# Performance work log

Measured on AMD Instinct MI355X. Metric: run time of the kernel, lower is better.

## Reference

```python
import jax, jax.numpy as jnp
import numpy as np

N, E, G, H = 100000, 1600000, 256, 2
EPS = 1e-5


def _gat_conv(x, src, dst, W, a_src, a_dst, bias, C):
    # PyG GATConv (concat=True, negative_slope=0.2): lin has no bias, bias added after concat.
    h = (x @ W).reshape(N, H, C)                                   # [N,H,C]
    e_src = (h * a_src).sum(-1)                                    # [N,H]
    e_dst = (h * a_dst).sum(-1)                                    # [N,H]
    alpha = jax.nn.leaky_relu(e_src[src] + e_dst[dst], 0.2)        # [Etot,H]
    amax = jax.ops.segment_max(alpha, dst, num_segments=N)         # segment softmax over incoming edges
    ex = jnp.exp(alpha - amax[dst])
    denom = jax.ops.segment_sum(ex, dst, num_segments=N)
    msg = h[src] * ex[:, :, None]                                  # [Etot,H,C]
    out = jax.ops.segment_sum(msg, dst, num_segments=N) / (denom[:, :, None] + 1e-16)
    return out.reshape(N, H * C) + bias


def _bn(x, g, b, m, v):  # BatchNorm in eval mode with running stats
    return g * (x - m) * jax.lax.rsqrt(v + EPS) + b


def _forward(edge_index, batch, x, w1, as1, ad1, b1, g1, be1, m1, v1, p1w, p1b,
             w2, as2, ad2, b2, g2, be2, m2, v2, p2w, p2b,
             w3, as3, ad3, b3, g3, be3, m3, v3, p3w, p3b,
             fw, fb, g4, be4, m4, v4, l1w, l1b, l2w, l2b):
    loops = jnp.arange(N, dtype=edge_index.dtype)                  # GATConv add_self_loops=True
    src = jnp.concatenate([edge_index[0], loops])
    dst = jnp.concatenate([edge_index[1], loops])
    h = jax.nn.relu(_bn(_gat_conv(x, src, dst, w1, as1, ad1, b1, 32), g1, be1, m1, v1)) + (x @ p1w + p1b)
    h = jax.nn.relu(_bn(_gat_conv(h, src, dst, w2, as2, ad2, b2, 64), g2, be2, m2, v2)) + (h @ p2w + p2b)
    h = jax.nn.relu(_bn(_gat_conv(h, src, dst, w3, as3, ad3, b3, 64), g3, be3, m3, v3)) + (h @ p3w + p3b)
    counts = jax.ops.segment_sum(jnp.ones((N,), h.dtype), batch, num_segments=G)
    pooled = jax.ops.segment_sum(h, batch, num_segments=G) / jnp.maximum(counts, 1.0)[:, None]  # [G,128]
    z = jax.nn.relu(_bn(pooled @ fw + fb, g4, be4, m4, v4))
    z = jax.nn.relu(z @ l1w + l1b)
    return z @ l2w + l2b                                           # [G,10]


def setup_inputs():
    key = jax.random.key(0)
    ks = jax.random.split(key, 48)
    it = iter(range(48))
    def rn(shape, s=0.1):
        return jax.random.normal(ks[next(it)], shape, jnp.float32) * s
    def bn_params(dim):  # gamma, beta, running_mean, running_var
        return (jax.random.uniform(ks[next(it)], (dim,), jnp.float32, 0.5, 1.5),
                rn((dim,)), rn((dim,)),
                jax.random.uniform(ks[next(it)], (dim,), jnp.float32, 0.5, 1.5))
    inp = {}
    inp["x"] = jax.random.normal(ks[next(it)], (N, 5), jnp.float32)
    inp["edge_index"] = jax.random.randint(ks[next(it)], (2, E), 0, N, jnp.int32)
    inp["batch"] = jnp.sort(jax.random.randint(ks[next(it)], (N,), 0, G, jnp.int32))
    inp["w1"], inp["as1"], inp["ad1"], inp["b1"] = rn((5, 64)), rn((H, 32)), rn((H, 32)), rn((64,))
    inp["g1"], inp["be1"], inp["m1"], inp["v1"] = bn_params(64)
    inp["p1w"], inp["p1b"] = rn((5, 64)), rn((64,))
    inp["w2"], inp["as2"], inp["ad2"], inp["b2"] = rn((64, 128)), rn((H, 64)), rn((H, 64)), rn((128,))
    inp["g2"], inp["be2"], inp["m2"], inp["v2"] = bn_params(128)
    inp["p2w"], inp["p2b"] = rn((64, 128)), rn((128,))
    inp["w3"], inp["as3"], inp["ad3"], inp["b3"] = rn((128, 128)), rn((H, 64)), rn((H, 64)), rn((128,))
    inp["g3"], inp["be3"], inp["m3"], inp["v3"] = bn_params(128)
    inp["p3w"], inp["p3b"] = rn((128, 128)), rn((128,))
    inp["fw"], inp["fb"] = rn((128, 32)), rn((32,))
    inp["g4"], inp["be4"], inp["m4"], inp["v4"] = bn_params(32)
    inp["l1w"], inp["l1b"] = rn((32, 32)), rn((32,))
    inp["l2w"], inp["l2b"] = rn((32, 10)), rn((10,))
    return inp


def reference(x, edge_index, batch, w1, as1, ad1, b1, g1, be1, m1, v1, p1w, p1b,
              w2, as2, ad2, b2, g2, be2, m2, v2, p2w, p2b,
              w3, as3, ad3, b3, g3, be3, m3, v3, p3w, p3b,
              fw, fb, g4, be4, m4, v4, l1w, l1b, l2w, l2b):
    return _forward(edge_index, batch, x, w1, as1, ad1, b1, g1, be1, m1, v1, p1w, p1b,
                    w2, as2, ad2, b2, g2, be2, m2, v2, p2w, p2b,
                    w3, as3, ad3, b3, g3, be3, m3, v3, p3w, p3b,
                    fw, fb, g4, be4, m4, v4, l1w, l1b, l2w, l2b)
```

## Files before the change

### kernel.cpp

```cpp
#include <hip/hip_runtime.h>
#include <hip/hip_bf16.h>
#include <hip/hip_fp16.h>

#define NN   100000
#define EE   1600000
#define ETOT (EE + NN)
#define GG   256
#define BNEPS 1e-5f
#define NBK  391
#define PADTOT (ETOT + NBK * 4096 + 64)
#define PSPLIT 16

typedef float floatx2 __attribute__((ext_vector_type(2)));
typedef short s16x8 __attribute__((ext_vector_type(8)));
typedef float f32x4v __attribute__((ext_vector_type(4)));

__device__ __forceinline__ unsigned short f2bf(float f) {
    unsigned u = __float_as_uint(f);
    unsigned r = u + 0x7FFF + ((u >> 16) & 1);
    return (unsigned short)(r >> 16);
}
__device__ __forceinline__ float bf2f(unsigned short b) {
    return __uint_as_float(((unsigned)b) << 16);
}
__device__ __forceinline__ floatx2 pkfma(floatx2 a, floatx2 b, floatx2 c) {
    return __builtin_elementwise_fma(a, b, c);
}


__global__ __launch_bounds__(256) void bucket_count_kernel(
    const int* __restrict__ ei, int* __restrict__ bucket_cnt)
{
    __shared__ int cnt[NBK];
    for (int i = threadIdx.x; i < NBK; i += 256) cnt[i] = 0;
    __syncthreads();
    int base = blockIdx.x * 8192;
    for (int k = threadIdx.x; k < 8192; k += 256) {
        int e = base + k;
        if (e < ETOT) {
            int dst = (e < EE) ? ei[EE + e] : (e - EE);
            atomicAdd(&cnt[dst >> 8], 1);
        }
    }
    __syncthreads();
    for (int i = threadIdx.x; i < NBK; i += 256)
        if (cnt[i]) atomicAdd(&bucket_cnt[i], cnt[i]);
}

__global__ __launch_bounds__(512) void bucket_scan_kernel(
    const int* __restrict__ bucket_cnt, int* __restrict__ bucket_base,
    int* __restrict__ gcursor, float* __restrict__ esrcs)
{
    __shared__ int s[512];
    int t = threadIdx.x;
    int v = (t < NBK) ? bucket_cnt[t] : 0;
    s[t] = v;
    __syncthreads();
    int x = v;
    for (int o = 1; o < 512; o <<= 1) {
        int y = (t >= o) ? s[t - o] : 0;
        __syncthreads();
        x += y;
        s[t] = x;
        __syncthreads();
    }
    if (t < NBK) { bucket_base[t] = x - v; gcursor[t] = x - v; }
    if (t == 0) {
        bucket_base[NBK] = ETOT;
        esrcs[2 * NN]     = __int_as_float(0xFF800000);
        esrcs[2 * NN + 1] = __int_as_float(0xFF800000);
    }
}

__global__ __launch_bounds__(256) void partition_kernel(
    const int* __restrict__ ei, int* __restrict__ gcursor, int* __restrict__ part)
{
    __shared__ int cnt[NBK];
    __shared__ int basel[NBK];
    for (int i = threadIdx.x; i < NBK; i += 256) cnt[i] = 0;
    __syncthreads();
    int base = blockIdx.x * 4096;
    for (int k = threadIdx.x; k < 4096; k += 256) {
        int e = base + k;
        if (e < ETOT) {
            int dst = (e < EE) ? ei[EE + e] : (e - EE);
            atomicAdd(&cnt[dst >> 8], 1);
        }
    }
    __syncthreads();
    for (int i = threadIdx.x; i < NBK; i += 256) {
        int c = cnt[i];
        basel[i] = c ? atomicAdd(&gcursor[i], c) : 0;
        cnt[i] = 0;
    }
    __syncthreads();
    for (int k = threadIdx.x; k < 4096; k += 256) {
        int e = base + k;
        if (e < ETOT) {
            int src, dst;
            if (e < EE) { src = ei[e]; dst = ei[EE + e]; }
            else        { src = e - EE; dst = e - EE; }
            int b = dst >> 8;
            int slot = atomicAdd(&cnt[b], 1);
            part[basel[b] + slot] = src | ((dst & 255) << 17);
        }
    }
}

__global__ __launch_bounds__(256) void csr_build_kernel(
    const int* __restrict__ part, const int* __restrict__ bucket_base,
    int* __restrict__ row2_start, int* __restrict__ row2_deg,
    int* __restrict__ csr2_src)
{
    __shared__ int degs[256];
    __shared__ int sc[256];
    __shared__ int cur[256];
    int b = blockIdx.x;
    int t = threadIdx.x;
    int beg = bucket_base[b], end = bucket_base[b + 1];
    int pbase = ((beg + 7) & ~7) + 4096 * b;
    degs[t] = 0;
    __syncthreads();
    for (int j = beg + t; j < end; j += 256)
        atomicAdd(&degs[(part[j] >> 17) & 255], 1);
    __syncthreads();
    int dg = degs[t];
    int pdeg = (dg + 7) & ~7;
    sc[t] = pdeg;
    __syncthreads();
    int x = pdeg;
    for (int o = 1; o < 256; o <<= 1) {
        int y = (t >= o) ? sc[t - o] : 0;
        __syncthreads();
        x += y;
        sc[t] = x;
        __syncthreads();
    }
    int start2 = pbase + (x - pdeg);
    int node = b * 256 + t;
    if (node < NN) { row2_start[node] = start2; row2_deg[node] = dg; }
    cur[t] = start2;
    __syncthreads();
    for (int j = beg + t; j < end; j += 256) {
        int pv = part[j];
        int pos = atomicAdd(&cur[(pv >> 17) & 255], 1);
        csr2_src[pos] = pv & 0x1FFFF;
    }
    for (int k = dg; k < pdeg; ++k) csr2_src[start2 + k] = NN;
}


template<int K>
__device__ __forceinline__ void prep_w_body(
    int unit, const float* __restrict__ W, const float* __restrict__ pw,
    short* __restrict__ wfrag)
{
    constexpr int KS = K / 32;
    int total = 16 * KS * 2 * 64;
    if (unit >= total) return;
    int lane = unit & 63;
    int rest = unit >> 6;
    int hilo = rest & 1;
    int fk = rest >> 1;
    int ks = fk % KS;
    int nt = fk / KS;
    int n = nt * 16 + (lane & 15);
    int k0 = ks * 32 + (lane >> 4) * 8;
    const float* src = (n < 128) ? (W + n) : (pw + (n - 128));
    s16x8 out;
#pragma unroll
    for (int j = 0; j < 8; ++j) {
        float wv = src[(size_t)(k0 + j) * 128];
        unsigned short hi = f2bf(wv);
        if (hilo == 0) {
            out[j] = (short)hi;
        } else {
            float fhi = __uint_as_float(((unsigned)hi) << 16);
            out[j] = (short)f2bf(wv - fhi);
        }
    }
    *(s16x8*)(wfrag + (size_t)unit * 8) = out;
}

__global__ __launch_bounds__(256) void prep_all_kernel(
    const float* __restrict__ w2, const float* __restrict__ p2w, short* __restrict__ wfrag2,
    const float* __restrict__ w3, const float* __restrict__ p3w, short* __restrict__ wfrag3,
    const float* b1, const float* g1, const float* be1, const float* m1, const float* v1,
    const float* b2, const float* g2, const float* be2, const float* m2, const float* v2,
    const float* b3, const float* g3, const float* be3, const float* m3, const float* v3,
    float* sc1, float* sh1, float* sc2, float* sh2, float* sc3, float* sh3)
{
    int b = blockIdx.x;
    int tid = threadIdx.x;
    if (b < 16) {
        prep_w_body<64>(b * 256 + tid, w2, p2w, wfrag2);
    } else if (b < 48) {
        prep_w_body<128>((b - 16) * 256 + tid, w3, p3w, wfrag3);
    } else {
        int t = tid;
        if (t < 128) {
            if (t < 64) {
                float sc = g1[t] * rsqrtf(v1[t] + BNEPS);
                sc1[t] = sc;
                sh1[t] = (b1[t] - m1[t]) * sc + be1[t];
            }
            {
                float sc = g2[t] * rsqrtf(v2[t] + BNEPS);
                sc2[t] = sc;
                sh2[t] = (b2[t] - m2[t]) * sc + be2[t];
            }
            {
                float sc = g3[t] * rsqrtf(v3[t] + BNEPS);
                sc3[t] = sc;
                sh3[t] = (b3[t] - m3[t]) * sc + be3[t];
            }
        }
    }
}


__global__ __launch_bounds__(256) void edgew_kernel(
    const int* __restrict__ csr2_src, const int* __restrict__ row2_start,
    const int* __restrict__ row2_deg,
    const float2* __restrict__ esrc, const float2* __restrict__ edst,
    unsigned* __restrict__ csr_w, int nN)
{
    int n = blockIdx.x * 4 + (threadIdx.x >> 6);
    int lane = threadIdx.x & 63;
    if (n >= nN) return;
    float2 ed = edst[n];
    int s2 = row2_start[n];
    int dg = row2_deg[n];
    int pc = (dg + 7) & ~7;
    for (int j = lane; j < pc; j += 64) {
        int i = csr2_src[s2 + j];
        float2 es = esrc[i];
        float a0 = es.x + ed.x; a0 = (a0 > 0.f) ? a0 : 0.2f * a0;
        float a1 = es.y + ed.y; a1 = (a1 > 0.f) ? a1 : 0.2f * a1;
        unsigned w = (unsigned)f2bf(__expf(a0)) | ((unsigned)f2bf(__expf(a1)) << 16);
        csr_w[s2 + j] = w;
    }
}


__global__ __launch_bounds__(256) void feat1_kernel(
    const float* __restrict__ xin, const float* __restrict__ W,
    const float* __restrict__ pw, const float* __restrict__ pb,
    const float* __restrict__ a_src, const float* __restrict__ a_dst,
    unsigned char* __restrict__ h8, float* __restrict__ esrc, float* __restrict__ edst,
    unsigned short* __restrict__ rout16, int nN)
{
    constexpr int F_IN = 5, F_OUT = 64;
    int t = threadIdx.x;
    int n = blockIdx.x * 4 + t / F_OUT;
    int f = t % F_OUT;
    if (n >= nN) return;
    float acc = 0.f, racc = 0.f;
#pragma unroll
    for (int k = 0; k < F_IN; ++k) {
        float xv = xin[n * F_IN + k];
        acc  += xv * W[k * F_OUT + f];
        racc += xv * pw[k * F_OUT + f];
    }
    float other = __shfl_xor(acc, 1, 64);
    if ((f & 1) == 0) {
        int p = __builtin_amdgcn_cvt_pk_fp8_f32(acc, other, 0, false);
        *(unsigned short*)(h8 + (size_t)n * F_OUT + f) = (unsigned short)(p & 0xFFFF);
    }
    rout16[(size_t)n * F_OUT + f] = f2bf(racc + pb[f]);
    float es = acc * a_src[f];
    float ed = acc * a_dst[f];
#pragma unroll
    for (int off = 16; off > 0; off >>= 1) {
        es += __shfl_xor(es, off, 32);
        ed += __shfl_xor(ed, off, 32);
    }
    if ((t & 31) == 0) {
        int head = (f >> 5) & 1;
        esrc[n * 2 + head] = es;
        edst[n * 2 + head] = ed;
    }
}


template<int K>
__global__ __launch_bounds__(512) void mfma_feat_kernel(
    const unsigned short* __restrict__ xin16, const short* __restrict__ wfrag,
    const float* __restrict__ pb,
    const float* __restrict__ a_src, const float* __restrict__ a_dst,
    unsigned char* __restrict__ h8, float* __restrict__ esrc, float* __restrict__ edst,
    unsigned short* __restrict__ rout16)
{
    constexpr int KS = K / 32;
    constexpr int CH = K / 8;
    __shared__ __align__(16) char smem[53248];
    s16x8* xs = (s16x8*)smem;
    unsigned short* h8lds = (unsigned short*)smem;
    unsigned short* rolds = (unsigned short*)(smem + 18432);

    const int tid = threadIdx.x;
    const int base = blockIdx.x * 128;

    for (int idx = tid; idx < 128 * CH; idx += 512) {
        int node = idx / CH;
        int ch = idx % CH;
        int gn = base + node; if (gn > NN - 1) gn = NN - 1;
        s16x8 v = *(const s16x8*)(xin16 + (size_t)gn * K + ch * 8);
        int tt = node >> 4, mm = node & 15;
        xs[(tt * CH + ch) * 16 + mm] = v;
    }
    __syncthreads();

    const int w = tid >> 6;
    const int lane = tid & 63;
    const int quad = lane >> 4;
    const int m = lane & 15;
    const int l0 = w * 16 + quad * 4;
    const int node0 = base + l0;

    s16x8 a0[KS];
#pragma unroll
    for (int ks = 0; ks < KS; ++ks)
        a0[ks] = xs[(w * CH + (ks * 4 + quad)) * 16 + m];
    __syncthreads();

    float esh0[4] = {0.f,0.f,0.f,0.f}, esh1[4] = {0.f,0.f,0.f,0.f};
    float edh0[4] = {0.f,0.f,0.f,0.f}, edh1[4] = {0.f,0.f,0.f,0.f};

#pragma unroll
    for (int nt = 0; nt < 16; ++nt) {
        s16x8 b[2 * KS];
#pragma unroll
        for (int i = 0; i < 2 * KS; ++i)
            b[i] = *(const s16x8*)(wfrag + (size_t)((nt * KS * 2 + i) * 64 + lane) * 8);
        f32x4v c0 = {0.f, 0.f, 0.f, 0.f};
#pragma unroll
        for (int ks = 0; ks < KS; ++ks) {
            c0 = __builtin_amdgcn_mfma_f32_16x16x32_bf16(a0[ks], b[2 * ks + 0], c0, 0, 0, 0);
            c0 = __builtin_amdgcn_mfma_f32_16x16x32_bf16(a0[ks], b[2 * ks + 1], c0, 0, 0, 0);
        }
        if (nt < 8) {
            int col = nt * 16 + m;
            float av = a_src[col], dv = a_dst[col];
#pragma unroll
            for (int r = 0; r < 4; ++r) {
                float v0 = c0[r];
                if (nt < 4) {
                    esh0[r] = fmaf(v0, av, esh0[r]); edh0[r] = fmaf(v0, dv, edh0[r]);
                } else {
                    esh1[r] = fmaf(v0, av, esh1[r]); edh1[r] = fmaf(v0, dv, edh1[r]);
                }
                float p0 = __shfl_xor(v0, 1, 16);
                if ((m & 1) == 0) {
                    int us = nt * 8 + (m >> 1);
                    int pk0 = __builtin_amdgcn_cvt_pk_fp8_f32(v0, p0, 0, false);
                    h8lds[(l0 + r) * 72 + us] = (unsigned short)(pk0 & 0xFFFF);
                }
            }
        } else {
            int col = (nt - 8) * 16 + m;
            float bv = pb[col];
#pragma unroll
            for (int r = 0; r < 4; ++r)
                rolds[(l0 + r) * 136 + col] = f2bf(c0[r] + bv);
        }
    }

#pragma unroll
    for (int r = 0; r < 4; ++r) {
#pragma unroll
        for (int off = 8; off > 0; off >>= 1) {
            esh0[r] += __shfl_xor(esh0[r], off, 16);
            esh1[r] += __shfl_xor(esh1[r], off, 16);
            edh0[r] += __shfl_xor(edh0[r], off, 16);
            edh1[r] += __shfl_xor(edh1[r], off, 16);
        }
    }
    if (m == 0) {
#pragma unroll
        for (int r = 0; r < 4; ++r) {
            if (node0 + r < NN) {
                ((float2*)esrc)[node0 + r] = make_float2(esh0[r], esh1[r]);
                ((float2*)edst)[node0 + r] = make_float2(edh0[r], edh1[r]);
            }
        }
    }

    __syncthreads();
    for (int i = tid; i < 128 * 8; i += 512) {
        int row = i >> 3, ch = i & 7;
        int node = base + row;
        if (node < NN) {
            int4 v = *(const int4*)(smem + row * 144 + ch * 16);
            *(int4*)(h8 + (size_t)node * 128 + ch * 16) = v;
        }
    }
    for (int i = tid; i < 128 * 16; i += 512) {
        int row = i >> 4, ch = i & 15;
        int node = base + row;
        if (node < NN) {
            int4 v = *(const int4*)(smem + 18432 + row * 272 + ch * 16);
            *(int4*)((char*)rout16 + (size_t)node * 256 + ch * 16) = v;
        }
    }
}


__global__ __launch_bounds__(256) void aggregate128_kernel(
    const unsigned char* __restrict__ h8,
    const int* __restrict__ row2_start, const int* __restrict__ row2_deg,
    const int* __restrict__ csr2_src, const unsigned* __restrict__ csr_w,
    const float* __restrict__ bnsc, const float* __restrict__ bnsh,
    unsigned short* __restrict__ io16)
{
    int w = threadIdx.x >> 6;
    int lane = threadIdx.x & 63;
    int half = lane >> 5;
    int fl = lane & 31;
    unsigned shl = (fl >= 16) ? 0u : 16u;
    int n = blockIdx.x * 8 + w * 2 + half;
    int s2 = row2_start[n];
    int dg = row2_deg[n];
    int pc = (dg + 7) & ~7;
    const int4* sp = (const int4*)(csr2_src + s2);
    const uint4* wp = (const uint4*)(csr_w + s2);
    float s = 0.f;
    floatx2 acc01 = {0.f, 0.f}, acc23 = {0.f, 0.f};
    for (int j = 0; j < pc; j += 8) {
        int4 ia = sp[(j >> 2) + 0];
        int4 ib = sp[(j >> 2) + 1];
        uint4 wa = wp[(j >> 2) + 0];
        uint4 wb = wp[(j >> 2) + 1];
        unsigned d0 = *(const unsigned*)(h8 + (size_t)ia.x * 128 + fl * 4);
        unsigned d1 = *(const unsigned*)(h8 + (size_t)ia.y * 128 + fl * 4);
        unsigned d2 = *(const unsigned*)(h8 + (size_t)ia.z * 128 + fl * 4);
        unsigned d3 = *(const unsigned*)(h8 + (size_t)ia.w * 128 + fl * 4);
        unsigned d4 = *(const unsigned*)(h8 + (size_t)ib.x * 128 + fl * 4);
        unsigned d5 = *(const unsigned*)(h8 + (size_t)ib.y * 128 + fl * 4);
        unsigned d6 = *(const unsigned*)(h8 + (size_t)ib.z * 128 + fl * 4);
        unsigned d7 = *(const unsigned*)(h8 + (size_t)ib.w * 128 + fl * 4);
        float g0 = __uint_as_float((wa.x << shl) & 0xFFFF0000u);
        float g1 = __uint_as_float((wa.y << shl) & 0xFFFF0000u);
        float g2 = __uint_as_float((wa.z << shl) & 0xFFFF0000u);
        float g3 = __uint_as_float((wa.w << shl) & 0xFFFF0000u);
        float g4 = __uint_as_float((wb.x << shl) & 0xFFFF0000u);
        float g5 = __uint_as_float((wb.y << shl) & 0xFFFF0000u);
        float g6 = __uint_as_float((wb.z << shl) & 0xFFFF0000u);
        float g7 = __uint_as_float((wb.w << shl) & 0xFFFF0000u);
        floatx2 gv0 = {g0, g0};
        floatx2 gv1 = {g1, g1};
        floatx2 gv2 = {g2, g2};
        floatx2 gv3 = {g3, g3};
        floatx2 gv4 = {g4, g4};
        floatx2 gv5 = {g5, g5};
        floatx2 gv6 = {g6, g6};
        floatx2 gv7 = {g7, g7};
        acc01 = pkfma(gv0, __builtin_amdgcn_cvt_pk_f32_fp8((int)d0, false), acc01);
        acc23 = pkfma(gv0, __builtin_amdgcn_cvt_pk_f32_fp8((int)d0, true),  acc23);
        acc01 = pkfma(gv1, __builtin_amdgcn_cvt_pk_f32_fp8((int)d1, false), acc01);
        acc23 = pkfma(gv1, __builtin_amdgcn_cvt_pk_f32_fp8((int)d1, true),  acc23);
        acc01 = pkfma(gv2, __builtin_amdgcn_cvt_pk_f32_fp8((int)d2, false), acc01);
        acc23 = pkfma(gv2, __builtin_amdgcn_cvt_pk_f32_fp8((int)d2, true),  acc23);
        acc01 = pkfma(gv3, __builtin_amdgcn_cvt_pk_f32_fp8((int)d3, false), acc01);
        acc23 = pkfma(gv3, __builtin_amdgcn_cvt_pk_f32_fp8((int)d3, true),  acc23);
        acc01 = pkfma(gv4, __builtin_amdgcn_cvt_pk_f32_fp8((int)d4, false), acc01);
        acc23 = pkfma(gv4, __builtin_amdgcn_cvt_pk_f32_fp8((int)d4, true),  acc23);
        acc01 = pkfma(gv5, __builtin_amdgcn_cvt_pk_f32_fp8((int)d5, false), acc01);
        acc23 = pkfma(gv5, __builtin_amdgcn_cvt_pk_f32_fp8((int)d5, true),  acc23);
        acc01 = pkfma(gv6, __builtin_amdgcn_cvt_pk_f32_fp8((int)d6, false), acc01);
        acc23 = pkfma(gv6, __builtin_amdgcn_cvt_pk_f32_fp8((int)d6, true),  acc23);
        acc01 = pkfma(gv7, __builtin_amdgcn_cvt_pk_f32_fp8((int)d7, false), acc01);
        acc23 = pkfma(gv7, __builtin_amdgcn_cvt_pk_f32_fp8((int)d7, true),  acc23);
        s += (((g0 + g1) + (g2 + g3)) + ((g4 + g5) + (g6 + g7)));
    }
    float inv = 1.f / (s + 1e-16f);
    int f0 = fl * 4;
    float4 sc = *(const float4*)(bnsc + f0);
    float4 sh = *(const float4*)(bnsh + f0);
    float o0 = fmaf(acc01.x * inv, sc.x, sh.x);
    float o1 = fmaf(acc01.y * inv, sc.y, sh.y);
    float o2 = fmaf(acc23.x * inv, sc.z, sh.z);
    float o3 = fmaf(acc23.y * inv, sc.w, sh.w);
    uint2* iop = (uint2*)(io16 + (size_t)n * 128 + f0);
    uint2 pu = *iop;
    float r0 = fmaxf(o0, 0.f) + __uint_as_float((pu.x & 0xFFFFu) << 16);
    float r1 = fmaxf(o1, 0.f) + __uint_as_float(pu.x & 0xFFFF0000u);
    float r2 = fmaxf(o2, 0.f) + __uint_as_float((pu.y & 0xFFFFu) << 16);
    float r3 = fmaxf(o3, 0.f) + __uint_as_float(pu.y & 0xFFFF0000u);
    uint2 ov;
    ov.x = (unsigned)f2bf(r0) | ((unsigned)f2bf(r1) << 16);
    ov.y = (unsigned)f2bf(r2) | ((unsigned)f2bf(r3) << 16);
    *iop = ov;
}


__global__ __launch_bounds__(256) void aggregate64_kernel(
    const unsigned char* __restrict__ h8,
    const int* __restrict__ row2_start, const int* __restrict__ row2_deg,
    const int* __restrict__ csr2_src, const unsigned* __restrict__ csr_w,
    const float* __restrict__ bnsc, const float* __restrict__ bnsh,
    unsigned short* __restrict__ io16)
{
    int w = threadIdx.x >> 6;
    int lane = threadIdx.x & 63;
    int half = lane >> 5;
    int hl = lane & 31;
    int q  = hl >> 4;
    int fl = hl & 15;
    unsigned shl = (fl >= 8) ? 0u : 16u;
    int n = blockIdx.x * 8 + w * 2 + half;
    int s2 = row2_start[n];
    int dg = row2_deg[n];
    int pc = (dg + 7) & ~7;
    const int4* sp = (const int4*)(csr2_src + s2);
    const uint4* wp = (const uint4*)(csr_w + s2);
    float s = 0.f;
    floatx2 acc01 = {0.f, 0.f}, acc23 = {0.f, 0.f};
    for (int j = 0; j < pc; j += 8) {
        int4 ia = sp[(j >> 2) + 0];
        int4 ib = sp[(j >> 2) + 1];
        uint4 wa = wp[(j >> 2) + 0];
        uint4 wb = wp[(j >> 2) + 1];
        int i0 = q ? ia.y : ia.x;
        int i1 = q ? ia.w : ia.z;
        int i2 = q ? ib.y : ib.x;
        int i3 = q ? ib.w : ib.z;
        unsigned w0 = q ? wa.y : wa.x;
        unsigned w1 = q ? wa.w : wa.z;
        unsigned w2 = q ? wb.y : wb.x;
        unsigned w3 = q ? wb.w : wb.z;
        unsigned d0 = *(const unsigned*)(h8 + (size_t)i0 * 64 + fl * 4);
        unsigned d1 = *(const unsigned*)(h8 + (size_t)i1 * 64 + fl * 4);
        unsigned d2 = *(const unsigned*)(h8 + (size_t)i2 * 64 + fl * 4);
        unsigned d3 = *(const unsigned*)(h8 + (size_t)i3 * 64 + fl * 4);
        float g0 = __uint_as_float((w0 << shl) & 0xFFFF0000u);
        float g1 = __uint_as_float((w1 << shl) & 0xFFFF0000u);
        float g2 = __uint_as_float((w2 << shl) & 0xFFFF0000u);
        float g3 = __uint_as_float((w3 << shl) & 0xFFFF0000u);
        floatx2 gv0 = {g0, g0};
        floatx2 gv1 = {g1, g1};
        floatx2 gv2 = {g2, g2};
        floatx2 gv3 = {g3, g3};
        acc01 = pkfma(gv0, __builtin_amdgcn_cvt_pk_f32_fp8((int)d0, false), acc01);
        acc23 = pkfma(gv0, __builtin_amdgcn_cvt_pk_f32_fp8((int)d0, true),  acc23);
        acc01 = pkfma(gv1, __builtin_amdgcn_cvt_pk_f32_fp8((int)d1, false), acc01);
        acc23 = pkfma(gv1, __builtin_amdgcn_cvt_pk_f32_fp8((int)d1, true),  acc23);
        acc01 = pkfma(gv2, __builtin_amdgcn_cvt_pk_f32_fp8((int)d2, false), acc01);
        acc23 = pkfma(gv2, __builtin_amdgcn_cvt_pk_f32_fp8((int)d2, true),  acc23);
        acc01 = pkfma(gv3, __builtin_amdgcn_cvt_pk_f32_fp8((int)d3, false), acc01);
        acc23 = pkfma(gv3, __builtin_amdgcn_cvt_pk_f32_fp8((int)d3, true),  acc23);
        s += ((g0 + g1) + (g2 + g3));
    }
    acc01.x += __shfl_xor(acc01.x, 16);
    acc01.y += __shfl_xor(acc01.y, 16);
    acc23.x += __shfl_xor(acc23.x, 16);
    acc23.y += __shfl_xor(acc23.y, 16);
    s += __shfl_xor(s, 16);
    if (hl < 16) {
        float inv = 1.f / (s + 1e-16f);
        int f0 = fl * 4;
        float4 sc = *(const float4*)(bnsc + f0);
        float4 sh = *(const float4*)(bnsh + f0);
        float o0 = fmaf(acc01.x * inv, sc.x, sh.x);
        float o1 = fmaf(acc01.y * inv, sc.y, sh.y);
        float o2 = fmaf(acc23.x * inv, sc.z, sh.z);
        float o3 = fmaf(acc23.y * inv, sc.w, sh.w);
        uint2* iop = (uint2*)(io16 + (size_t)n * 64 + f0);
        uint2 pu = *iop;
        float r0 = fmaxf(o0, 0.f) + __uint_as_float((pu.x & 0xFFFFu) << 16);
        float r1 = fmaxf(o1, 0.f) + __uint_as_float(pu.x & 0xFFFF0000u);
        float r2 = fmaxf(o2, 0.f) + __uint_as_float((pu.y & 0xFFFFu) << 16);
        float r3 = fmaxf(o3, 0.f) + __uint_as_float(pu.y & 0xFFFF0000u);
        uint2 ov;
        ov.x = (unsigned)f2bf(r0) | ((unsigned)f2bf(r1) << 16);
        ov.y = (unsigned)f2bf(r2) | ((unsigned)f2bf(r3) << 16);
        *iop = ov;
    }
}


__global__ __launch_bounds__(128) void pool_partial_kernel(
    const unsigned short* __restrict__ hf16, const int* __restrict__ batch,
    float* __restrict__ ppart)
{
    int g = blockIdx.x / PSPLIT;
    int p = blockIdx.x % PSPLIT;
    int f = threadIdx.x;
    int lo = 0, hi = NN;
    while (lo < hi) { int mid = (lo + hi) >> 1; if (batch[mid] < g) lo = mid + 1; else hi = mid; }
    int start = lo;
    hi = NN;
    while (lo < hi) { int mid = (lo + hi) >> 1; if (batch[mid] < g + 1) lo = mid + 1; else hi = mid; }
    int end = lo;
    int len = end - start;
    int chunk = (len + PSPLIT - 1) / PSPLIT;
    int i0 = start + p * chunk;
    int i1 = i0 + chunk; if (i1 > end) i1 = end;
    float acc = 0.f;
    for (int i = i0; i < i1; ++i) acc += bf2f(hf16[(size_t)i * 128 + f]);
    ppart[((size_t)g * PSPLIT + p) * 128 + f] = acc;
}


__global__ __launch_bounds__(128) void head_kernel(
    const float* __restrict__ ppart, const int* __restrict__ batch,
    const float* __restrict__ fw, const float* __restrict__ fb,
    const float* __restrict__ g4, const float* __restrict__ be4,
    const float* __restrict__ m4, const float* __restrict__ v4,
    const float* __restrict__ l1w, const float* __restrict__ l1b,
    const float* __restrict__ l2w, const float* __restrict__ l2b,
    float* __restrict__ out)
{
    __shared__ float p[128];
    __shared__ float z1[32];
    __shared__ float z2[32];
    int g = blockIdx.x, t = threadIdx.x;
    int lo = 0, hi = NN;
    while (lo < hi) { int mid = (lo + hi) >> 1; if (batch[mid] < g) lo = mid + 1; else hi = mid; }
    int start = lo;
    hi = NN;
    while (lo < hi) { int mid = (lo + hi) >> 1; if (batch[mid] < g + 1) lo = mid + 1; else hi = mid; }
    float cnt = (float)(lo - start);
    float acc = 0.f;
#pragma unroll
    for (int q = 0; q < PSPLIT; ++q)
        acc += ppart[((size_t)g * PSPLIT + q) * 128 + t];
    p[t] = acc / fmaxf(cnt, 1.0f);
    __syncthreads();
    if (t < 32) {
        float a = fb[t];
        for (int k = 0; k < 128; ++k) a += p[k] * fw[k * 32 + t];
        float val = g4[t] * (a - m4[t]) * rsqrtf(v4[t] + BNEPS) + be4[t];
        z1[t] = fmaxf(val, 0.f);
    }
    __syncthreads();
    if (t < 32) {
        float a = l1b[t];
        for (int k = 0; k < 32; ++k) a += z1[k] * l1w[k * 32 + t];
        z2[t] = fmaxf(a, 0.f);
    }
    __syncthreads();
    if (t < 10) {
        float a = l2b[t];
        for (int k = 0; k < 32; ++k) a += z2[k] * l2w[k * 10 + t];
        out[g * 10 + t] = a;
    }
}


extern "C" void kernel_launch(void* const* d_in, const int* in_sizes, int n_in,
                              void* d_out, int out_size, void* d_ws, size_t ws_size,
                              hipStream_t stream) {
    const float* x     = (const float*)d_in[0];
    const int*   ei    = (const int*)d_in[1];
    const int*   batch = (const int*)d_in[2];
    const float* w1  = (const float*)d_in[3];
    const float* as1 = (const float*)d_in[4];
    const float* ad1 = (const float*)d_in[5];
    const float* b1  = (const float*)d_in[6];
    const float* g1  = (const float*)d_in[7];
    const float* be1 = (const float*)d_in[8];
    const float* m1  = (const float*)d_in[9];
    const float* v1  = (const float*)d_in[10];
    const float* p1w = (const float*)d_in[11];
    const float* p1b = (const float*)d_in[12];
    const float* w2  = (const float*)d_in[13];
    const float* as2 = (const float*)d_in[14];
    const float* ad2 = (const float*)d_in[15];
    const float* b2  = (const float*)d_in[16];
    const float* g2  = (const float*)d_in[17];
    const float* be2 = (const float*)d_in[18];
    const float* m2  = (const float*)d_in[19];
    const float* v2  = (const float*)d_in[20];
    const float* p2w = (const float*)d_in[21];
    const float* p2b = (const float*)d_in[22];
    const float* w3  = (const float*)d_in[23];
    const float* as3 = (const float*)d_in[24];
    const float* ad3 = (const float*)d_in[25];
    const float* b3  = (const float*)d_in[26];
    const float* g3  = (const float*)d_in[27];
    const float* be3 = (const float*)d_in[28];
    const float* m3  = (const float*)d_in[29];
    const float* v3  = (const float*)d_in[30];
    const float* p3w = (const float*)d_in[31];
    const float* p3b = (const float*)d_in[32];
    const float* fw  = (const float*)d_in[33];
    const float* fb  = (const float*)d_in[34];
    const float* g4  = (const float*)d_in[35];
    const float* be4 = (const float*)d_in[36];
    const float* m4  = (const float*)d_in[37];
    const float* v4  = (const float*)d_in[38];
    const float* l1w = (const float*)d_in[39];
    const float* l1b = (const float*)d_in[40];
    const float* l2w = (const float*)d_in[41];
    const float* l2b = (const float*)d_in[42];

    char* ws = (char*)d_ws;
    size_t off = 0;
    auto alloc = [&](size_t bytes) -> char* {
        char* p = ws + off;
        off += (bytes + 255) & ~(size_t)255;
        return p;
    };
    int*    bucket_cnt  = (int*)alloc((NBK) * sizeof(int));
    int*    bucket_base = (int*)alloc((NBK + 1) * sizeof(int));
    int*    gcursor     = (int*)alloc((NBK) * sizeof(int));
    int*    part        = (int*)alloc((size_t)ETOT * sizeof(int));
    int*    row2_start  = (int*)alloc(NN * sizeof(int));
    int*    row2_deg    = (int*)alloc(NN * sizeof(int));
    int*    csr2_src    = (int*)alloc((size_t)PADTOT * sizeof(int));
    unsigned* csr_w     = (unsigned*)alloc((size_t)PADTOT * sizeof(unsigned));
    unsigned char*  h8  = (unsigned char*)alloc((size_t)(NN + 1) * 128);
    unsigned short* hb1 = (unsigned short*)alloc((size_t)NN * 64 * sizeof(short));
    unsigned short* hb2 = (unsigned short*)alloc((size_t)NN * 128 * sizeof(short));
    unsigned short* hb3 = (unsigned short*)alloc((size_t)NN * 128 * sizeof(short));
    float*  esrc        = (float*)alloc((size_t)(NN + 1) * 2 * sizeof(float));
    float*  edst        = (float*)alloc((size_t)NN * 2 * sizeof(float));
    float*  ppart       = (float*)alloc((size_t)GG * PSPLIT * 128 * sizeof(float));
    short*  wfrag2      = (short*)alloc((size_t)16 * 2 * 2 * 64 * 8 * sizeof(short));
    short*  wfrag3      = (short*)alloc((size_t)16 * 4 * 2 * 64 * 8 * sizeof(short));
    float*  bnsc1       = (float*)alloc(64 * sizeof(float));
    float*  bnsh1       = (float*)alloc(64 * sizeof(float));
    float*  bnsc2       = (float*)alloc(128 * sizeof(float));
    float*  bnsh2       = (float*)alloc(128 * sizeof(float));
    float*  bnsc3       = (float*)alloc(128 * sizeof(float));
    float*  bnsh3       = (float*)alloc(128 * sizeof(float));

    prep_all_kernel<<<49, 256, 0, stream>>>(
        w2, p2w, wfrag2, w3, p3w, wfrag3,
        b1, g1, be1, m1, v1, b2, g2, be2, m2, v2, b3, g3, be3, m3, v3,
        bnsc1, bnsh1, bnsc2, bnsh2, bnsc3, bnsh3);

    hipMemsetAsync(bucket_cnt, 0, NBK * sizeof(int), stream);
    bucket_count_kernel<<<(ETOT + 8191) / 8192, 256, 0, stream>>>(ei, bucket_cnt);
    bucket_scan_kernel<<<1, 512, 0, stream>>>(bucket_cnt, bucket_base, gcursor, esrc);
    partition_kernel<<<(ETOT + 4095) / 4096, 256, 0, stream>>>(ei, gcursor, part);
    csr_build_kernel<<<NBK, 256, 0, stream>>>(part, bucket_base, row2_start, row2_deg, csr2_src);

    feat1_kernel<<<(NN + 3) / 4, 256, 0, stream>>>(
        x, w1, p1w, p1b, as1, ad1, h8, esrc, edst, hb1, NN);
    edgew_kernel<<<(NN + 3) / 4, 256, 0, stream>>>(
        csr2_src, row2_start, row2_deg, (const float2*)esrc, (const float2*)edst, csr_w, NN);
    aggregate64_kernel<<<NN / 8, 256, 0, stream>>>(
        h8, row2_start, row2_deg, csr2_src, csr_w, bnsc1, bnsh1, hb1);

    mfma_feat_kernel<64><<<(NN + 127) / 128, 512, 0, stream>>>(
        hb1, wfrag2, p2b, as2, ad2, h8, esrc, edst, hb2);
    edgew_kernel<<<(NN + 3) / 4, 256, 0, stream>>>(
        csr2_src, row2_start, row2_deg, (const float2*)esrc, (const float2*)edst, csr_w, NN);
    aggregate128_kernel<<<NN / 8, 256, 0, stream>>>(
        h8, row2_start, row2_deg, csr2_src, csr_w, bnsc2, bnsh2, hb2);

    mfma_feat_kernel<128><<<(NN + 127) / 128, 512, 0, stream>>>(
        hb2, wfrag3, p3b, as3, ad3, h8, esrc, edst, hb3);
    edgew_kernel<<<(NN + 3) / 4, 256, 0, stream>>>(
        csr2_src, row2_start, row2_deg, (const float2*)esrc, (const float2*)edst, csr_w, NN);
    aggregate128_kernel<<<NN / 8, 256, 0, stream>>>(
        h8, row2_start, row2_deg, csr2_src, csr_w, bnsc3, bnsh3, hb3);

    pool_partial_kernel<<<GG * PSPLIT, 128, 0, stream>>>(hb3, batch, ppart);
    head_kernel<<<GG, 128, 0, stream>>>(ppart, batch, fw, fb, g4, be4, m4, v4,
                                        l1w, l1b, l2w, l2b, (float*)d_out);
}
```

Baseline: 502.9 us.

## Restructure MFMA feature GEMM so each wave holds weight tiles across row tiles

The MFMA feature kernel now processes 64 nodes per block instead of 128. Each wave keeps two output column tiles of weights in registers and loops over four row tiles, so weight fragments are loaded once rather than reloaded for each of 16 column tiles. Attention logit partials are reduced per column tile and combined through shared memory, and the shared allocation shrinks, with a launch bound asking for four blocks per CU. The cost is twice as many blocks, a cross-wave reduction step, and possible register pressure from holding both weight tiles.

Result: faster. 488.8 us (-2.8%).

```diff
diff --git a/kernel.cpp b/kernel.cpp
--- a/kernel.cpp
+++ b/kernel.cpp
@@ -284,7 +284,7 @@
 
 
 template<int K>
-__global__ __launch_bounds__(512) void mfma_feat_kernel(
+__global__ __launch_bounds__(512, 4) void mfma_feat_kernel(
     const unsigned short* __restrict__ xin16, const short* __restrict__ wfrag,
     const float* __restrict__ pb,
     const float* __restrict__ a_src, const float* __restrict__ a_dst,
@@ -293,15 +293,16 @@
 {
     constexpr int KS = K / 32;
     constexpr int CH = K / 8;
-    __shared__ __align__(16) char smem[53248];
+    __shared__ __align__(16) char smem[1024 * CH + 28672];
     s16x8* xs = (s16x8*)smem;
-    unsigned short* h8lds = (unsigned short*)smem;
-    unsigned short* rolds = (unsigned short*)(smem + 18432);
+    unsigned short* h8lds = (unsigned short*)(smem + 1024 * CH);
+    unsigned short* rolds = (unsigned short*)(smem + 1024 * CH + 9216);
+    float2* espart = (float2*)(smem + 1024 * CH + 26624);
 
     const int tid = threadIdx.x;
-    const int base = blockIdx.x * 128;
-
-    for (int idx = tid; idx < 128 * CH; idx += 512) {
+    const int base = blockIdx.x * 64;
+
+    for (int idx = tid; idx < 64 * CH; idx += 512) {
         int node = idx / CH;
         int ch = idx % CH;
         int gn = base + node; if (gn > NN - 1) gn = NN - 1;
@@ -315,91 +316,96 @@
     const int lane = tid & 63;
     const int quad = lane >> 4;
     const int m = lane & 15;
-    const int l0 = w * 16 + quad * 4;
-    const int node0 = base + l0;
-
-    s16x8 a0[KS];
-#pragma unroll
-    for (int ks = 0; ks < KS; ++ks)
-        a0[ks] = xs[(w * CH + (ks * 4 + quad)) * 16 + m];
-    __syncthreads();
-
-    float esh0[4] = {0.f,0.f,0.f,0.f}, esh1[4] = {0.f,0.f,0.f,0.f};
-    float edh0[4] = {0.f,0.f,0.f,0.f}, edh1[4] = {0.f,0.f,0.f,0.f};
-
-#pragma unroll
-    for (int nt = 0; nt < 16; ++nt) {
-        s16x8 b[2 * KS];
-#pragma unroll
-        for (int i = 0; i < 2 * KS; ++i)
-            b[i] = *(const s16x8*)(wfrag + (size_t)((nt * KS * 2 + i) * 64 + lane) * 8);
-        f32x4v c0 = {0.f, 0.f, 0.f, 0.f};
+    const int nt0 = 2 * w, nt1 = nt0 + 1;
+
+    s16x8 bA[2 * KS], bB[2 * KS];
+#pragma unroll
+    for (int i = 0; i < 2 * KS; ++i) {
+        bA[i] = *(const s16x8*)(wfrag + (size_t)((nt0 * KS * 2 + i) * 64 + lane) * 8);
+        bB[i] = *(const s16x8*)(wfrag + (size_t)((nt1 * KS * 2 + i) * 64 + lane) * 8);
+    }
+
+    const bool hpart = (w < 4);
+    float av0 = 0.f, dv0 = 0.f, av1 = 0.f, dv1 = 0.f, bv0 = 0.f, bv1 = 0.f;
+    if (hpart) {
+        av0 = a_src[nt0 * 16 + m]; dv0 = a_dst[nt0 * 16 + m];
+        av1 = a_src[nt1 * 16 + m]; dv1 = a_dst[nt1 * 16 + m];
+    } else {
+        bv0 = pb[(nt0 - 8) * 16 + m]; bv1 = pb[(nt1 - 8) * 16 + m];
+    }
+
+#pragma unroll
+    for (int rt = 0; rt < 4; ++rt) {
+        s16x8 a[KS];
+#pragma unroll
+        for (int ks = 0; ks < KS; ++ks)
+            a[ks] = xs[(rt * CH + ks * 4 + quad) * 16 + m];
+        f32x4v cA = {0.f, 0.f, 0.f, 0.f};
+        f32x4v cB = {0.f, 0.f, 0.f, 0.f};
 #pragma unroll
         for (int ks = 0; ks < KS; ++ks) {
-            c0 = __builtin_amdgcn_mfma_f32_16x16x32_bf16(a0[ks], b[2 * ks + 0], c0, 0, 0, 0);
-            c0 = __builtin_amdgcn_mfma_f32_16x16x32_bf16(a0[ks], b[2 * ks + 1], c0, 0, 0, 0);
-        }
-        if (nt < 8) {
-            int col = nt * 16 + m;
-            float av = a_src[col], dv = a_dst[col];
+            cA = __builtin_amdgcn_mfma_f32_16x16x32_bf16(a[ks], bA[2 * ks + 0], cA, 0, 0, 0);
+            cA = __builtin_amdgcn_mfma_f32_16x16x32_bf16(a[ks], bA[2 * ks + 1], cA, 0, 0, 0);
+            cB = __builtin_amdgcn_mfma_f32_16x16x32_bf16(a[ks], bB[2 * ks + 0], cB, 0, 0, 0);
+            cB = __builtin_amdgcn_mfma_f32_16x16x32_bf16(a[ks], bB[2 * ks + 1], cB, 0, 0, 0);
+        }
+        int row0 = rt * 16 + quad * 4;
+        if (hpart) {
 #pragma unroll
             for (int r = 0; r < 4; ++r) {
-                float v0 = c0[r];
-                if (nt < 4) {
-                    esh0[r] = fmaf(v0, av, esh0[r]); edh0[r] = fmaf(v0, dv, edh0[r]);
-                } else {
-                    esh1[r] = fmaf(v0, av, esh1[r]); edh1[r] = fmaf(v0, dv, edh1[r]);
+                float v0 = cA[r], v1 = cB[r];
+                float es = v0 * av0 + v1 * av1;
+                float ed = v0 * dv0 + v1 * dv1;
+#pragma unroll
+                for (int off = 8; off > 0; off >>= 1) {
+                    es += __shfl_xor(es, off, 16);
+                    ed += __shfl_xor(ed, off, 16);
                 }
+                if (m == 0) espart[w * 64 + row0 + r] = make_float2(es, ed);
                 float p0 = __shfl_xor(v0, 1, 16);
+                float p1 = __shfl_xor(v1, 1, 16);
                 if ((m & 1) == 0) {
-                    int us = nt * 8 + (m >> 1);
                     int pk0 = __builtin_amdgcn_cvt_pk_fp8_f32(v0, p0, 0, false);
-                    h8lds[(l0 + r) * 72 + us] = (unsigned short)(pk0 & 0xFFFF);
+                    int pk1 = __builtin_amdgcn_cvt_pk_fp8_f32(v1, p1, 0, false);
+                    h8lds[(row0 + r) * 72 + nt0 * 8 + (m >> 1)] = (unsigned short)(pk0 & 0xFFFF);
+                    h8lds[(row0 + r) * 72 + nt1 * 8 + (m >> 1)] = (unsigned short)(pk1 & 0xFFFF);
                 }
             }
         } else {
-            int col = (nt - 8) * 16 + m;
-            float bv = pb[col];
-#pragma unroll
-            for (int r = 0; r < 4; ++r)
-                rolds[(l0 + r) * 136 + col] = f2bf(c0[r] + bv);
-        }
-    }
-
-#pragma unroll
-    for (int r = 0; r < 4; ++r) {
-#pragma unroll
-        for (int off = 8; off > 0; off >>= 1) {
-            esh0[r] += __shfl_xor(esh0[r], off, 16);
-            esh1[r] += __shfl_xor(esh1[r], off, 16);
-            edh0[r] += __shfl_xor(edh0[r], off, 16);
-            edh1[r] += __shfl_xor(edh1[r], off, 16);
-        }
-    }
-    if (m == 0) {
-#pragma unroll
-        for (int r = 0; r < 4; ++r) {
-            if (node0 + r < NN) {
-                ((float2*)esrc)[node0 + r] = make_float2(esh0[r], esh1[r]);
-                ((float2*)edst)[node0 + r] = make_float2(edh0[r], edh1[r]);
+#pragma unroll
+            for (int r = 0; r < 4; ++r) {
+                rolds[(row0 + r) * 136 + (nt0 - 8) * 16 + m] = f2bf(cA[r] + bv0);
+                rolds[(row0 + r) * 136 + (nt1 - 8) * 16 + m] = f2bf(cB[r] + bv1);
             }
         }
     }
 
     __syncthreads();
-    for (int i = tid; i < 128 * 8; i += 512) {
+
+    if (tid < 64) {
+        int node = base + tid;
+        if (node < NN) {
+            float2 e0 = espart[0 * 64 + tid];
+            float2 e1 = espart[1 * 64 + tid];
+            float2 e2 = espart[2 * 64 + tid];
+            float2 e3 = espart[3 * 64 + tid];
+            ((float2*)esrc)[node] = make_float2(e0.x + e1.x, e2.x + e3.x);
+            ((float2*)edst)[node] = make_float2(e0.y + e1.y, e2.y + e3.y);
+        }
+    }
+    for (int i = tid; i < 64 * 8; i += 512) {
         int row = i >> 3, ch = i & 7;
         int node = base + row;
         if (node < NN) {
-            int4 v = *(const int4*)(smem + row * 144 + ch * 16);
+            int4 v = *(const int4*)((char*)h8lds + row * 144 + ch * 16);
             *(int4*)(h8 + (size_t)node * 128 + ch * 16) = v;
         }
     }
-    for (int i = tid; i < 128 * 16; i += 512) {
+    for (int i = tid; i < 64 * 16; i += 512) {
         int row = i >> 4, ch = i & 15;
         int node = base + row;
         if (node < NN) {
-            int4 v = *(const int4*)(smem + 18432 + row * 272 + ch * 16);
+            int4 v = *(const int4*)((char*)rolds + row * 272 + ch * 16);
             *(int4*)((char*)rout16 + (size_t)node * 256 + ch * 16) = v;
         }
     }
@@ -744,14 +750,14 @@
     aggregate64_kernel<<<NN / 8, 256, 0, stream>>>(
         h8, row2_start, row2_deg, csr2_src, csr_w, bnsc1, bnsh1, hb1);
 
-    mfma_feat_kernel<64><<<(NN + 127) / 128, 512, 0, stream>>>(
+    mfma_feat_kernel<64><<<(NN + 63) / 64, 512, 0, stream>>>(
         hb1, wfrag2, p2b, as2, ad2, h8, esrc, edst, hb2);
     edgew_kernel<<<(NN + 3) / 4, 256, 0, stream>>>(
         csr2_src, row2_start, row2_deg, (const float2*)esrc, (const float2*)edst, csr_w, NN);
     aggregate128_kernel<<<NN / 8, 256, 0, stream>>>(
         h8, row2_start, row2_deg, csr2_src, csr_w, bnsc2, bnsh2, hb2);
 
-    mfma_feat_kernel<128><<<(NN + 127) / 128, 512, 0, stream>>>(
+    mfma_feat_kernel<128><<<(NN + 63) / 64, 512, 0, stream>>>(
         hb2, wfrag3, p3b, as3, ad3, h8, esrc, edst, hb3);
     edgew_kernel<<<(NN + 3) / 4, 256, 0, stream>>>(
         csr2_src, row2_start, row2_deg, (const float2*)esrc, (const float2*)edst, csr_w, NN);
```
